# Kernel optimization log

Hardware: AMD Instinct MI355X
Metric: run time of the kernel (lower is better)

## Reference

```python
import jax, jax.numpy as jnp
import numpy as np

N_HEAD = 16


def setup_inputs() -> dict:
    key = jax.random.key(0)
    ks = jax.random.split(key, 6)
    B, T, C = 2, 2048, 1024
    hs = C // N_HEAD  # 64
    block_minus_1 = 2048  # block_size - 1
    x = jax.random.normal(ks[0], (B, T, C), dtype=jnp.float32)
    W1 = jax.random.normal(ks[1], (C, C), dtype=jnp.float32) * (1.0 / np.sqrt(C))
    b1 = jnp.zeros((C,), dtype=jnp.float32)
    # original init: uniform(-1e-3, 1e-3)
    w2 = jax.random.uniform(ks[2], (hs, block_minus_1), dtype=jnp.float32, minval=-1e-3, maxval=1e-3)
    b2 = jnp.zeros((block_minus_1,), dtype=jnp.float32)
    Wv = jax.random.normal(ks[3], (C, C), dtype=jnp.float32) * (1.0 / np.sqrt(C))
    bv = jnp.zeros((C,), dtype=jnp.float32)
    Wp = jax.random.normal(ks[4], (C, C), dtype=jnp.float32) * (1.0 / np.sqrt(C))
    bp = jnp.zeros((C,), dtype=jnp.float32)
    return {"x": x, "W1": W1, "b1": b1, "w2": w2, "b2": b2,
            "Wv": Wv, "bv": bv, "Wp": Wp, "bp": bp}


def reference(x, W1, b1, w2, b2, Wv, bv, Wp, bp):
    B, T, C = x.shape
    hs = C // N_HEAD
    r = jax.nn.relu(x @ W1.T + b1).reshape(B, T, N_HEAD, hs).transpose(0, 2, 1, 3)
    # synthesizer scores: (B, nh, T, T) = relu_out @ w2[:, :T] + b2[:T]
    att = jnp.einsum('bhtd,dj->bhtj', r, w2[:, :T]) + b2[:T]
    causal = jnp.tril(jnp.ones((T, T), dtype=bool))
    att = jnp.where(causal[None, None], att, jnp.float32(-1e10))
    att = jax.nn.softmax(att, axis=-1)  # attn_drop = 0 (eval)
    v = (x @ Wv.T + bv).reshape(B, T, N_HEAD, hs).transpose(0, 2, 1, 3)
    y = jnp.einsum('bhtj,bhjd->bhtd', att, v)
    y = y.transpose(0, 2, 1, 3).reshape(B, T, C)
    return y @ Wp.T + bp  # resid_drop = 0 (eval)
```

## Files before the change

kernel.cpp:

```cpp
#include <hip/hip_runtime.h>

typedef __bf16 bf16x8 __attribute__((ext_vector_type(8)));
typedef float f32x4 __attribute__((ext_vector_type(4)));

__device__ __forceinline__ unsigned short f2bf(float f) {
  union { float f; unsigned u; } v; v.f = f;
  unsigned u = v.u;
  return (unsigned short)((u + 0x7fffu + ((u >> 16) & 1u)) >> 16);
}
__device__ __forceinline__ unsigned short f2bf_fast(float f) {
  union { float f; unsigned u; } v; v.f = f;
  return (unsigned short)((v.u + 0x8000u) >> 16);
}
__device__ __forceinline__ void gload_lds16(const void* g, void* l) {
  __builtin_amdgcn_global_load_lds(
      (const __attribute__((address_space(1))) unsigned int*)g,
      (__attribute__((address_space(3))) unsigned int*)l, 16, 0, 0);
}
__device__ __forceinline__ void cvt4(const float* __restrict__ s,
                                     unsigned short* __restrict__ d, int u) {
  f32x4 v = ((const f32x4*)s)[u];
  union { unsigned short s[4]; unsigned long long u; } o;
  o.s[0] = f2bf(v[0]); o.s[1] = f2bf(v[1]); o.s[2] = f2bf(v[2]); o.s[3] = f2bf(v[3]);
  ((unsigned long long*)d)[u] = o.u;
}


__global__ void prep(const float* __restrict__ x, const float* __restrict__ W1,
                     const float* __restrict__ Wv, const float* __restrict__ Wp,
                     const float* __restrict__ w2, const float* __restrict__ b2,
                     unsigned short* __restrict__ xb, unsigned short* __restrict__ W1b,
                     unsigned short* __restrict__ Wvb, unsigned short* __restrict__ Wpb,
                     unsigned short* __restrict__ w2t, unsigned short* __restrict__ ebj) {
  int u = blockIdx.x * 256 + threadIdx.x;
  if (u < 1048576) { cvt4(x, xb, u); return; }
  u -= 1048576;
  if (u < 262144) { cvt4(W1, W1b, u); return; }
  u -= 262144;
  if (u < 262144) { cvt4(Wv, Wvb, u); return; }
  u -= 262144;
  if (u < 262144) { cvt4(Wp, Wpb, u); return; }
  u -= 262144;
  if (u < 32768) {
    int j = u >> 4, d4 = (u & 15) * 4;
    union { unsigned short s[4]; unsigned long long x; } o;
#pragma unroll
    for (int i = 0; i < 4; ++i) o.s[i] = f2bf(w2[(d4 + i) * 2048 + j]);
    ((unsigned long long*)w2t)[u] = o.x;
    return;
  }
  u -= 32768;
  union { unsigned short s[4]; unsigned long long x; } o;
#pragma unroll
  for (int i = 0; i < 4; ++i) o.s[i] = f2bf(__expf(b2[u * 4 + i]));
  ((unsigned long long*)ebj)[u] = o.x;
}

__global__ __launch_bounds__(256) void gemm_rv(
    const unsigned short* __restrict__ xb, const unsigned short* __restrict__ W1b,
    const unsigned short* __restrict__ Wvb, const float* __restrict__ b1,
    const float* __restrict__ bv, const float* __restrict__ b2,
    unsigned short* __restrict__ rb, unsigned short* __restrict__ vtb) {
  __shared__ unsigned short As[128 * 64];
  __shared__ unsigned short Bs[64 * 64];
  int id = blockIdx.x;
  const unsigned short *A, *Bt;
  const float* bias;
  unsigned short* C;
  int N, tileM, tileN, epi;
  if (id < 512) {
    A = xb; Bt = W1b; bias = b1; C = rb; N = 1024; epi = 0;
    tileN = (id & 15) * 64; tileM = (id >> 4) * 128;
  } else {
    id -= 512;
    A = Wvb; Bt = xb; bias = bv; C = vtb; N = 4096; epi = 1;
    tileN = (id & 63) * 64; tileM = (id >> 6) * 128;
  }
  const int tid = threadIdx.x;
  const int wv = tid >> 6, ln = tid & 63;
  const int quad = ln >> 4, lq = ln & 15;
  const int rowL = ln >> 3;
  const int kc = (((ln & 7) ^ rowL) & 7) * 8;
  const int sx = lq & 7;
  const int ko0 = (quad ^ sx) * 8, ko1 = ((4 + quad) ^ sx) * 8;

  f32x4 acc[2][4];
  const f32x4 zf = {0.f, 0.f, 0.f, 0.f};
#pragma unroll
  for (int i = 0; i < 2; ++i)
#pragma unroll
    for (int j = 0; j < 4; ++j) acc[i][j] = zf;

  for (int k0 = 0; k0 < 1024; k0 += 64) {
    __syncthreads();
#pragma unroll
    for (int l = 0; l < 4; ++l) {
      int row = l * 32 + wv * 8 + rowL;
      gload_lds16(A + (tileM + row) * 1024 + k0 + kc, &As[l * 2048 + wv * 512]);
    }
#pragma unroll
    for (int l = 0; l < 2; ++l) {
      int row = l * 32 + wv * 8 + rowL;
      gload_lds16(Bt + (tileN + row) * 1024 + k0 + kc, &Bs[l * 2048 + wv * 512]);
    }
    __syncthreads();
#pragma unroll
    for (int kk = 0; kk < 2; ++kk) {
      const int ko = kk ? ko1 : ko0;
      bf16x8 af[2], bfr[4];
#pragma unroll
      for (int mi = 0; mi < 2; ++mi)
        af[mi] = *(const bf16x8*)&As[(wv * 32 + mi * 16 + lq) * 64 + ko];
#pragma unroll
      for (int ni = 0; ni < 4; ++ni)
        bfr[ni] = *(const bf16x8*)&Bs[(ni * 16 + lq) * 64 + ko];
#pragma unroll
      for (int mi = 0; mi < 2; ++mi)
#pragma unroll
        for (int ni = 0; ni < 4; ++ni)
          acc[mi][ni] = __builtin_amdgcn_mfma_f32_16x16x32_bf16(af[mi], bfr[ni], acc[mi][ni], 0, 0, 0);
    }
  }
#pragma unroll
  for (int ni = 0; ni < 4; ++ni) {
    int col = tileN + ni * 16 + lq;
    float eb = (epi == 1) ? __expf(b2[col & 2047]) : 0.0f;
#pragma unroll
    for (int mi = 0; mi < 2; ++mi) {
#pragma unroll
      for (int rg = 0; rg < 4; ++rg) {
        int row = tileM + wv * 32 + mi * 16 + quad * 4 + rg;
        float v = acc[mi][ni][rg];
        if (epi == 0) {
          v += bias[col];
          v = v > 0.f ? v : 0.f;
        } else {
          v = (v + bias[row]) * eb;
        }
        C[row * N + col] = f2bf(v);
      }
    }
  }
}

__global__ __launch_bounds__(256) void gemm_p(
    const unsigned short* __restrict__ A, const unsigned short* __restrict__ Bt,
    const float* __restrict__ bias, float* __restrict__ C) {
  __shared__ unsigned short As[64 * 64];
  __shared__ unsigned short Bs[64 * 64];
  const int tid = threadIdx.x;
  const int wv = tid >> 6, ln = tid & 63;
  const int quad = ln >> 4, lq = ln & 15;
  const int tileM = blockIdx.y * 64, tileN = blockIdx.x * 64;
  const int rowL = ln >> 3;
  const int kc = (((ln & 7) ^ rowL) & 7) * 8;
  const int sx = lq & 7;
  const int ko0 = (quad ^ sx) * 8, ko1 = ((4 + quad) ^ sx) * 8;

  f32x4 acc[4];
  const f32x4 zf = {0.f, 0.f, 0.f, 0.f};
#pragma unroll
  for (int j = 0; j < 4; ++j) acc[j] = zf;

  for (int k0 = 0; k0 < 1024; k0 += 64) {
    __syncthreads();
#pragma unroll
    for (int l = 0; l < 2; ++l) {
      int row = l * 32 + wv * 8 + rowL;
      gload_lds16(A + (tileM + row) * 1024 + k0 + kc, &As[l * 2048 + wv * 512]);
      gload_lds16(Bt + (tileN + row) * 1024 + k0 + kc, &Bs[l * 2048 + wv * 512]);
    }
    __syncthreads();
#pragma unroll
    for (int kk = 0; kk < 2; ++kk) {
      const int ko = kk ? ko1 : ko0;
      bf16x8 af = *(const bf16x8*)&As[(wv * 16 + lq) * 64 + ko];
#pragma unroll
      for (int ni = 0; ni < 4; ++ni) {
        bf16x8 bfr = *(const bf16x8*)&Bs[(ni * 16 + lq) * 64 + ko];
        acc[ni] = __builtin_amdgcn_mfma_f32_16x16x32_bf16(af, bfr, acc[ni], 0, 0, 0);
      }
    }
  }
#pragma unroll
  for (int ni = 0; ni < 4; ++ni) {
    int col = tileN + ni * 16 + lq;
#pragma unroll
    for (int rg = 0; rg < 4; ++rg) {
      int row = tileM + wv * 16 + quad * 4 + rg;
      C[row * 1024 + col] = acc[ni][rg] + bias[col];
    }
  }
}

__global__ __launch_bounds__(256, 2) void attn(
    const unsigned short* __restrict__ r, const unsigned short* __restrict__ w2t,
    const unsigned short* __restrict__ vt, const unsigned short* __restrict__ ebj,
    unsigned short* __restrict__ y) {
  __shared__ unsigned short W2s[2][64 * 64];
  __shared__ unsigned short Vs[2][64 * 64];
  __shared__ unsigned short Ps[4][16 * 64];

  const int tid = threadIdx.x;
  const int wv = tid >> 6, ln = tid & 63;
  const int quad = ln >> 4, lq = ln & 15;
  const int p = blockIdx.x;
  const int bh = blockIdx.y, b = bh >> 4, h = bh & 15;
  const int ta = p, tb = 31 - p;
  const int t0a = ta * 64, t0b = tb * 64;
  const int rowL = ln >> 3;
  const int kc = (((ln & 7) ^ rowL) & 7) * 8;
  const int sx = lq & 7;
  const int ko0 = (quad ^ sx) * 8, ko1 = ((4 + quad) ^ sx) * 8;

  bf16x8 ra[2][2];
  {
    const unsigned short* base = r + (b * 2048 + wv * 16 + lq) * 1024 + h * 64 + quad * 8;
    ra[0][0] = *(const bf16x8*)(base + t0a * 1024);
    ra[0][1] = *(const bf16x8*)(base + t0a * 1024 + 32);
    ra[1][0] = *(const bf16x8*)(base + t0b * 1024);
    ra[1][1] = *(const bf16x8*)(base + t0b * 1024 + 32);
  }

  f32x4 accY[4];
  f32x4 accL;
  const f32x4 zf = {0.f, 0.f, 0.f, 0.f};
#pragma unroll
  for (int nd = 0; nd < 4; ++nd) accY[nd] = zf;
  accL = zf;

  auto stage = [&](int jt, int bi) {
    int j0 = jt * 64;
#pragma unroll
    for (int l = 0; l < 2; ++l) {
      int row = l * 32 + wv * 8 + rowL;
      gload_lds16(w2t + (j0 + row) * 64 + kc, &W2s[bi][l * 2048 + wv * 512]);
      gload_lds16(vt + (h * 64 + row) * 4096 + b * 2048 + j0 + kc,
                  &Vs[bi][l * 2048 + wv * 512]);
    }
  };

  stage(0, 0);
  for (int it = 0; it <= 32; ++it) {
    const int cb = it & 1;
    __syncthreads();
    if (it < 32) {
      int nit = it + 1;
      int njt = (nit <= p) ? nit : (nit - p - 1);
      stage(njt, cb ^ 1);
    }
    const int s = (it <= p) ? 0 : 1;
    const int jt = (it <= p) ? it : (it - p - 1);
    const int tts = s ? tb : ta;
    const int t0 = tts * 64;
    const int j0 = jt * 64;

    bf16x8 eb0 = *(const bf16x8*)&ebj[j0 + quad * 8];
    bf16x8 eb1 = *(const bf16x8*)&ebj[j0 + 32 + quad * 8];
    bf16x8 w2f0[4], w2f1[4];
#pragma unroll
    for (int ni = 0; ni < 4; ++ni) {
      w2f0[ni] = *(const bf16x8*)&W2s[cb][(ni * 16 + lq) * 64 + ko0];
      w2f1[ni] = *(const bf16x8*)&W2s[cb][(ni * 16 + lq) * 64 + ko1];
    }

    f32x4 sv[4] = {zf, zf, zf, zf};
#pragma unroll
    for (int ni = 0; ni < 4; ++ni) {
      sv[ni] = __builtin_amdgcn_mfma_f32_16x16x32_bf16(ra[s][0], w2f0[ni], sv[ni], 0, 0, 0);
      sv[ni] = __builtin_amdgcn_mfma_f32_16x16x32_bf16(ra[s][1], w2f1[ni], sv[ni], 0, 0, 0);
    }

    const bool diag = (jt == tts);
#pragma unroll
    for (int ni = 0; ni < 4; ++ni) {
      int j = j0 + ni * 16 + lq;
#pragma unroll
      for (int rg = 0; rg < 4; ++rg) {
        float pe = __expf(sv[ni][rg]);
        if (diag) {
          int t = t0 + wv * 16 + quad * 4 + rg;
          pe = (j <= t) ? pe : 0.f;
        }
        Ps[wv][(quad * 4 + rg) * 64 +
               (((ni * 2 + (lq >> 3)) ^ ((quad * 4 + rg) & 7)) * 8) + (lq & 7)] = f2bf_fast(pe);
      }
    }

#pragma unroll
    for (int kk = 0; kk < 2; ++kk) {
      const int ko = kk ? ko1 : ko0;
      bf16x8 pa = *(const bf16x8*)&Ps[wv][lq * 64 + ko];
#pragma unroll
      for (int nd = 0; nd < 4; ++nd) {
        bf16x8 bb = *(const bf16x8*)&Vs[cb][(nd * 16 + lq) * 64 + ko];
        accY[nd] = __builtin_amdgcn_mfma_f32_16x16x32_bf16(pa, bb, accY[nd], 0, 0, 0);
      }
      accL = __builtin_amdgcn_mfma_f32_16x16x32_bf16(pa, kk ? eb1 : eb0, accL, 0, 0, 0);
    }

    if (it == p || it == 32) {
      float inv[4];
#pragma unroll
      for (int rg = 0; rg < 4; ++rg) inv[rg] = __builtin_amdgcn_rcpf(accL[rg]);
#pragma unroll
      for (int nd = 0; nd < 4; ++nd)
#pragma unroll
        for (int rg = 0; rg < 4; ++rg) {
          int t = t0 + wv * 16 + quad * 4 + rg;
          y[(b * 2048 + t) * 1024 + h * 64 + nd * 16 + lq] = f2bf(accY[nd][rg] * inv[rg]);
        }
#pragma unroll
      for (int nd = 0; nd < 4; ++nd) accY[nd] = zf;
      accL = zf;
    }
  }
}

extern "C" void kernel_launch(void* const* d_in, const int* in_sizes, int n_in,
                              void* d_out, int out_size, void* d_ws, size_t ws_size,
                              hipStream_t stream) {
  const float* x  = (const float*)d_in[0];
  const float* W1 = (const float*)d_in[1];
  const float* b1 = (const float*)d_in[2];
  const float* w2 = (const float*)d_in[3];
  const float* b2 = (const float*)d_in[4];
  const float* Wv = (const float*)d_in[5];
  const float* bv = (const float*)d_in[6];
  const float* Wp = (const float*)d_in[7];
  const float* bp = (const float*)d_in[8];

  unsigned short* ws  = (unsigned short*)d_ws;
  unsigned short* xb   = ws;
  unsigned short* W1b  = ws + 4194304;
  unsigned short* Wvb  = ws + 5242880;
  unsigned short* Wpb  = ws + 6291456;
  unsigned short* w2t  = ws + 7340032;
  unsigned short* rb   = ws + 7471104;
  unsigned short* vt   = ws + 11665408;
  unsigned short* yb   = ws + 15859712;
  unsigned short* ebjb = ws + 20054016;

  prep<<<7298, 256, 0, stream>>>(x, W1, Wv, Wp, w2, b2, xb, W1b, Wvb, Wpb, w2t, ebjb);
  gemm_rv<<<1024, 256, 0, stream>>>(xb, W1b, Wvb, b1, bv, b2, rb, vt);
  attn<<<dim3(16, 32), 256, 0, stream>>>(rb, w2t, vt, ebjb, yb);
  gemm_p<<<dim3(16, 64), 256, 0, stream>>>(yb, Wpb, bp, (float*)d_out);
}
```

Before: 188.7 us.

## Fuse R and V projections into one block sharing the x tile

```diff
diff --git a/kernel.cpp b/kernel.cpp
--- a/kernel.cpp
+++ b/kernel.cpp
@@ -61,21 +61,10 @@
     const unsigned short* __restrict__ Wvb, const float* __restrict__ b1,
     const float* __restrict__ bv, const float* __restrict__ b2,
     unsigned short* __restrict__ rb, unsigned short* __restrict__ vtb) {
-  __shared__ unsigned short As[128 * 64];
-  __shared__ unsigned short Bs[64 * 64];
-  int id = blockIdx.x;
-  const unsigned short *A, *Bt;
-  const float* bias;
-  unsigned short* C;
-  int N, tileM, tileN, epi;
-  if (id < 512) {
-    A = xb; Bt = W1b; bias = b1; C = rb; N = 1024; epi = 0;
-    tileN = (id & 15) * 64; tileM = (id >> 4) * 128;
-  } else {
-    id -= 512;
-    A = Wvb; Bt = xb; bias = bv; C = vtb; N = 4096; epi = 1;
-    tileN = (id & 63) * 64; tileM = (id >> 6) * 128;
-  }
+  __shared__ unsigned short Xs[128 * 64];
+  __shared__ unsigned short W1s[64 * 64];
+  __shared__ unsigned short Wvs[64 * 64];
+  const int tm = blockIdx.x * 128, n0 = blockIdx.y * 64;
   const int tid = threadIdx.x;
   const int wv = tid >> 6, ln = tid & 63;
   const int quad = ln >> 4, lq = ln & 15;
@@ -84,61 +73,74 @@
   const int sx = lq & 7;
   const int ko0 = (quad ^ sx) * 8, ko1 = ((4 + quad) ^ sx) * 8;
 
-  f32x4 acc[2][4];
+  f32x4 accR[2][4];
+  f32x4 accV[8];
   const f32x4 zf = {0.f, 0.f, 0.f, 0.f};
 #pragma unroll
   for (int i = 0; i < 2; ++i)
 #pragma unroll
-    for (int j = 0; j < 4; ++j) acc[i][j] = zf;
+    for (int j = 0; j < 4; ++j) accR[i][j] = zf;
+#pragma unroll
+  for (int j = 0; j < 8; ++j) accV[j] = zf;
 
   for (int k0 = 0; k0 < 1024; k0 += 64) {
     __syncthreads();
 #pragma unroll
     for (int l = 0; l < 4; ++l) {
       int row = l * 32 + wv * 8 + rowL;
-      gload_lds16(A + (tileM + row) * 1024 + k0 + kc, &As[l * 2048 + wv * 512]);
+      gload_lds16(xb + (tm + row) * 1024 + k0 + kc, &Xs[l * 2048 + wv * 512]);
     }
 #pragma unroll
     for (int l = 0; l < 2; ++l) {
       int row = l * 32 + wv * 8 + rowL;
-      gload_lds16(Bt + (tileN + row) * 1024 + k0 + kc, &Bs[l * 2048 + wv * 512]);
+      gload_lds16(W1b + (n0 + row) * 1024 + k0 + kc, &W1s[l * 2048 + wv * 512]);
+      gload_lds16(Wvb + (n0 + row) * 1024 + k0 + kc, &Wvs[l * 2048 + wv * 512]);
     }
     __syncthreads();
 #pragma unroll
     for (int kk = 0; kk < 2; ++kk) {
       const int ko = kk ? ko1 : ko0;
-      bf16x8 af[2], bfr[4];
+      bf16x8 xa[2], w1f[4];
 #pragma unroll
       for (int mi = 0; mi < 2; ++mi)
-        af[mi] = *(const bf16x8*)&As[(wv * 32 + mi * 16 + lq) * 64 + ko];
+        xa[mi] = *(const bf16x8*)&Xs[(wv * 32 + mi * 16 + lq) * 64 + ko];
 #pragma unroll
       for (int ni = 0; ni < 4; ++ni)
-        bfr[ni] = *(const bf16x8*)&Bs[(ni * 16 + lq) * 64 + ko];
+        w1f[ni] = *(const bf16x8*)&W1s[(ni * 16 + lq) * 64 + ko];
 #pragma unroll
       for (int mi = 0; mi < 2; ++mi)
 #pragma unroll
         for (int ni = 0; ni < 4; ++ni)
-          acc[mi][ni] = __builtin_amdgcn_mfma_f32_16x16x32_bf16(af[mi], bfr[ni], acc[mi][ni], 0, 0, 0);
+          accR[mi][ni] = __builtin_amdgcn_mfma_f32_16x16x32_bf16(xa[mi], w1f[ni], accR[mi][ni], 0, 0, 0);
+      bf16x8 wva = *(const bf16x8*)&Wvs[(wv * 16 + lq) * 64 + ko];
+#pragma unroll
+      for (int nj = 0; nj < 8; ++nj) {
+        bf16x8 xbf = *(const bf16x8*)&Xs[(nj * 16 + lq) * 64 + ko];
+        accV[nj] = __builtin_amdgcn_mfma_f32_16x16x32_bf16(wva, xbf, accV[nj], 0, 0, 0);
+      }
     }
   }
 #pragma unroll
   for (int ni = 0; ni < 4; ++ni) {
-    int col = tileN + ni * 16 + lq;
-    float eb = (epi == 1) ? __expf(b2[col & 2047]) : 0.0f;
-#pragma unroll
-    for (int mi = 0; mi < 2; ++mi) {
+    int col = n0 + ni * 16 + lq;
+    float bc = b1[col];
+#pragma unroll
+    for (int mi = 0; mi < 2; ++mi)
 #pragma unroll
       for (int rg = 0; rg < 4; ++rg) {
-        int row = tileM + wv * 32 + mi * 16 + quad * 4 + rg;
-        float v = acc[mi][ni][rg];
-        if (epi == 0) {
-          v += bias[col];
-          v = v > 0.f ? v : 0.f;
-        } else {
-          v = (v + bias[row]) * eb;
-        }
-        C[row * N + col] = f2bf(v);
-      }
+        int row = tm + wv * 32 + mi * 16 + quad * 4 + rg;
+        float v = accR[mi][ni][rg] + bc;
+        rb[row * 1024 + col] = f2bf(v > 0.f ? v : 0.f);
+      }
+  }
+#pragma unroll
+  for (int nj = 0; nj < 8; ++nj) {
+    int tok = tm + nj * 16 + lq;
+    float eb = __expf(b2[tok & 2047]);
+#pragma unroll
+    for (int rg = 0; rg < 4; ++rg) {
+      int ch = n0 + wv * 16 + quad * 4 + rg;
+      vtb[ch * 4096 + tok] = f2bf((accV[nj][rg] + bv[ch]) * eb);
     }
   }
 }
@@ -204,8 +206,8 @@
   const int tid = threadIdx.x;
   const int wv = tid >> 6, ln = tid & 63;
   const int quad = ln >> 4, lq = ln & 15;
-  const int p = blockIdx.x;
-  const int bh = blockIdx.y, b = bh >> 4, h = bh & 15;
+  const int bh = blockIdx.x, b = bh >> 4, h = bh & 15;
+  const int p = blockIdx.y;
   const int ta = p, tb = 31 - p;
   const int t0a = ta * 64, t0b = tb * 64;
   const int rowL = ln >> 3;
@@ -342,7 +344,7 @@
   unsigned short* ebjb = ws + 20054016;
 
   prep<<<7298, 256, 0, stream>>>(x, W1, Wv, Wp, w2, b2, xb, W1b, Wvb, Wpb, w2t, ebjb);
-  gemm_rv<<<1024, 256, 0, stream>>>(xb, W1b, Wvb, b1, bv, b2, rb, vt);
-  attn<<<dim3(16, 32), 256, 0, stream>>>(rb, w2t, vt, ebjb, yb);
+  gemm_rv<<<dim3(32, 16), 256, 0, stream>>>(xb, W1b, Wvb, b1, bv, b2, rb, vt);
+  attn<<<dim3(32, 16), 256, 0, stream>>>(rb, w2t, vt, ebjb, yb);
   gemm_p<<<dim3(16, 64), 256, 0, stream>>>(yb, Wpb, bp, (float*)d_out);
 }
```

New measurement: 182.4 us. -3.3%, faster.
